# Optimization experiments

Measured on AMD Instinct MI355X. Metric: run time of the kernel, lower is better.

The kernel has to match this reference:

```python
import jax, jax.numpy as jnp
import numpy as np

DIM = 64
HEAD_DIM = 4
NUM_HEADS = DIM // HEAD_DIM  # 16
ATTN_DIM = NUM_HEADS * HEAD_DIM  # 64
BN_EPS = 1e-5


def setup_inputs() -> dict:
    key = jax.random.key(0)
    k_x, k_qkv, k_proj, k_g, k_b, k_m, k_v = jax.random.split(key, 7)
    B, C, H, W = 8, DIM, 64, 64
    x = jax.random.normal(k_x, (B, C, H, W), dtype=jnp.float32)
    # nn.Linear(dim, 3*attn_dim, bias=False): y = x @ W^T; store transposed for x @ w
    w_qkv = jax.random.normal(k_qkv, (DIM, 3 * ATTN_DIM), dtype=jnp.float32) * (DIM ** -0.5)
    w_proj = jax.random.normal(k_proj, (ATTN_DIM, DIM), dtype=jnp.float32) * (ATTN_DIM ** -0.5)
    gamma = 1.0 + 0.1 * jax.random.normal(k_g, (DIM,), dtype=jnp.float32)
    beta = 0.1 * jax.random.normal(k_b, (DIM,), dtype=jnp.float32)
    bn_mean = 0.1 * jax.random.normal(k_m, (DIM,), dtype=jnp.float32)
    bn_var = jnp.abs(jax.random.normal(k_v, (DIM,), dtype=jnp.float32)) + 0.5
    return {"x": x, "w_qkv": w_qkv, "w_proj": w_proj, "gamma": gamma,
            "beta": beta, "bn_mean": bn_mean, "bn_var": bn_var}


def _forward(x, w_qkv, w_proj, gamma, beta, bn_mean, bn_var):
    B, C, H, W = x.shape
    Hp, Wp = H // 2, W // 2
    N = Hp * Wp
    # ---- MaxPool2d(2,2) with indices (non-overlapping windows) ----
    xr = x.reshape(B, C, Hp, 2, Wp, 2).transpose(0, 1, 2, 4, 3, 5).reshape(B, C, Hp, Wp, 4)
    idx = jnp.argmax(xr, axis=-1)              # [B,C,Hp,Wp] window-local argmax
    pooled = jnp.max(xr, axis=-1)              # [B,C,Hp,Wp]
    # ---- GA attention on pooled map ----
    t = pooled.transpose(0, 2, 3, 1).reshape(B, N, C)          # [B,N,C]
    qkv = (t @ w_qkv).reshape(B, N, 3, NUM_HEADS, HEAD_DIM)
    q, k, v = qkv[:, :, 0], qkv[:, :, 1], qkv[:, :, 2]          # [B,N,h,d]
    scale = HEAD_DIM ** -0.5
    attn = jnp.einsum('bnhd,bmhd->bhnm', q, k) * scale          # [B,h,N,N]
    attn = jax.nn.softmax(attn, axis=-1)
    o = jnp.einsum('bhnm,bmhd->bnhd', attn, v).reshape(B, N, ATTN_DIM)
    o = (o @ w_proj).reshape(B, Hp, Wp, C).transpose(0, 3, 1, 2)  # [B,C,Hp,Wp]
    # ---- BatchNorm2d (eval mode, running stats) ----
    inv = gamma / jnp.sqrt(bn_var + BN_EPS)
    o = o * inv[:, None, None] + (beta - bn_mean * inv)[:, None, None]
    # ---- MaxUnpool2d(2,2): scatter to argmax positions ----
    oh = jax.nn.one_hot(idx, 4, dtype=o.dtype)                  # [B,C,Hp,Wp,4]
    up = oh * o[..., None]
    out = up.reshape(B, C, Hp, Wp, 2, 2).transpose(0, 1, 2, 4, 3, 5).reshape(B, C, H, W)
    return out


def reference(x, w_qkv, w_proj, gamma, beta, bn_mean, bn_var):
    return _forward(x, w_qkv, w_proj, gamma, beta, bn_mean, bn_var)
```

## Files before the change

kernel.cpp:

```cpp
#include <hip/hip_runtime.h>
#include <hip/hip_bf16.h>


typedef float    f32x4 __attribute__((ext_vector_type(4)));
typedef _Float16 f16x8 __attribute__((ext_vector_type(8)));
typedef unsigned int uint32_tt;

__global__ __launch_bounds__(256) void pool_kernel(const float* __restrict__ x,
                                                   float* __restrict__ t,
                                                   int* __restrict__ idx) {
    int g = blockIdx.x * 256 + threadIdx.x;
    int wp = g & 31, hp = (g >> 5) & 31, c = (g >> 10) & 63, b = g >> 16;
    const float* px = x + (((b * 64 + c) * 64 + 2 * hp) * 64 + 2 * wp);
    float2 r0 = *(const float2*)px;
    float2 r1 = *(const float2*)(px + 64);
    float best = r0.x; int bi = 0;
    if (r0.y > best) { best = r0.y; bi = 1; }
    if (r1.x > best) { best = r1.x; bi = 2; }
    if (r1.y > best) { best = r1.y; bi = 3; }
    int n = hp * 32 + wp;
    t[(b * 1024 + n) * 64 + c] = best;
    idx[g] = bi;
}

__global__ __launch_bounds__(192) void qkv_kernel(const float* __restrict__ t,
                                                  const float* __restrict__ w_qkv,
                                                  float* __restrict__ q,
                                                  float* __restrict__ k,
                                                  float* __restrict__ v) {
    __shared__ float trow[16 * 64];
    int tid = threadIdx.x;
    int row0 = blockIdx.x * 16;
    for (int i = tid; i < 1024; i += 192) trow[i] = t[row0 * 64 + i];
    int j  = tid % 96;
    int rh = tid / 96;
    float wc0[64], wc1[64];
    #pragma unroll
    for (int c = 0; c < 64; c++) {
        wc0[c] = w_qkv[c * 192 + j];
        wc1[c] = w_qkv[c * 192 + j + 96];
    }
    __syncthreads();
    int s0 = j >> 6, h0 = (j >> 2) & 15, d0 = j & 3;
    int j1 = j + 96;
    int s1 = j1 >> 6, h1 = (j1 >> 2) & 15, d1 = j1 & 3;
    float* dst0 = (s0 == 0) ? q : (s0 == 1) ? k : v;
    float* dst1 = (s1 == 0) ? q : (s1 == 1) ? k : v;
    for (int r = 0; r < 8; r++) {
        int row = rh * 8 + r;
        const float4* tr = (const float4*)&trow[row * 64];
        float a0 = 0.f, a1 = 0.f;
        #pragma unroll
        for (int c4 = 0; c4 < 16; c4++) {
            float4 tv = tr[c4];
            a0 += tv.x * wc0[c4 * 4] + tv.y * wc0[c4 * 4 + 1]
                + tv.z * wc0[c4 * 4 + 2] + tv.w * wc0[c4 * 4 + 3];
            a1 += tv.x * wc1[c4 * 4] + tv.y * wc1[c4 * 4 + 1]
                + tv.z * wc1[c4 * 4 + 2] + tv.w * wc1[c4 * 4 + 3];
        }
        int ng = row0 + row, b = ng >> 10, n = ng & 1023;
        dst0[((b * 16 + h0) * 1024 + n) * 4 + d0] = a0;
        dst1[((b * 16 + h1) * 1024 + n) * 4 + d1] = a1;
    }
}

__global__ __launch_bounds__(256) void attn_kernel(const float* __restrict__ q,
                                                   const float* __restrict__ k,
                                                   const float* __restrict__ v,
                                                   float* __restrict__ o) {
    __shared__ __align__(16) unsigned char smem[38080];
    f16x8*     Kh2 = (f16x8*)smem;
    uint32_tt* VT  = (uint32_tt*)(smem + 16384);
    float*     lsc = (float*)(smem + 37024);
    int bh = blockIdx.x >> 2;
    int row0 = (blockIdx.x & 3) * 256;
    int tid = threadIdx.x;
    const float4* kp4 = (const float4*)(k + bh * 4096);
    const float4* vp4 = (const float4*)(v + bh * 4096);
    #pragma unroll
    for (int i = 0; i < 4; i++) {
        int key = i * 256 + tid;
        float4 kf = kp4[key];
        f16x8 kk;
        kk[0] = (_Float16)kf.x; kk[4] = (_Float16)(kf.x - (float)kk[0]);
        kk[1] = (_Float16)kf.y; kk[5] = (_Float16)(kf.y - (float)kk[1]);
        kk[2] = (_Float16)kf.z; kk[6] = (_Float16)(kf.z - (float)kk[2]);
        kk[3] = (_Float16)kf.w; kk[7] = (_Float16)(kf.w - (float)kk[3]);
        Kh2[key] = kk;
        float4 vf = vp4[key];
        float vd[4] = { vf.x, vf.y, vf.z, vf.w };
        #pragma unroll
        for (int d = 0; d < 4; d++) {
            _Float16 h = (_Float16)vd[d];
            _Float16 l = (_Float16)(vd[d] - (float)h);
            uint32_tt hi = (uint32_tt)__builtin_bit_cast(unsigned short, l);
            uint32_tt lo = (uint32_tt)__builtin_bit_cast(unsigned short, h);
            VT[d * 1032 + key] = lo | (hi << 16);
        }
        VT[4 * 1032 + key] = 0x00003C00u;
    }
    int w = tid >> 6, lane = tid & 63;
    int c = lane & 15, quad = lane >> 4;
    int mv = (c < 5) ? c : 4;
    const float C1 = 0.5f * 1.44269504088896f;
    const float4* qp4 = (const float4*)(q + bh * 4096);
    f16x8 bq[4];
    #pragma unroll
    for (int s = 0; s < 4; s++) {
        int rowg = row0 + w * 64 + s * 16 + c;
        float4 qv = qp4[rowg];
        float qx = qv.x * C1, qy = qv.y * C1, qz = qv.z * C1, qw = qv.w * C1;
        _Float16 hx = (_Float16)qx, hy = (_Float16)qy,
                 hz = (_Float16)qz, hw = (_Float16)qw;
        _Float16 gx = (_Float16)(qx - (float)hx), gy = (_Float16)(qy - (float)hy),
                 gz = (_Float16)(qz - (float)hz), gw = (_Float16)(qw - (float)hw);
        f16x8 a = {};
        if (quad == 0) {
            a[0] = hx; a[1] = hy; a[2] = hz; a[3] = hw;
            a[4] = hx; a[5] = hy; a[6] = hz; a[7] = hw;
        } else if (quad == 1) {
            a[0] = gx; a[1] = gy; a[2] = gz; a[3] = gw;
            a[4] = gx; a[5] = gy; a[6] = gz; a[7] = gw;
        }
        bq[s] = a;
    }
    __syncthreads();
    f32x4 acc[4];
    #pragma unroll
    for (int s = 0; s < 4; s++) acc[s] = (f32x4)(0.f);
    #pragma unroll 2
    for (int t = 0; t < 64; t++) {
        f16x8 ka = Kh2[t * 16 + c];
        const uint32_tt* vp = &VT[mv * 1032 + t * 16 + quad * 4];
        uint4 vr = *(const uint4*)vp;
        f16x8 va = __builtin_bit_cast(f16x8, vr);
        #pragma unroll
        for (int s = 0; s < 4; s++) {
            f32x4 S = __builtin_amdgcn_mfma_f32_16x16x32_f16(ka, bq[s],
                                                             (f32x4)(0.f), 0, 0, 0);
            float p0 = __builtin_amdgcn_exp2f(S[0] - 14.f);
            float p1 = __builtin_amdgcn_exp2f(S[1] - 14.f);
            float p2 = __builtin_amdgcn_exp2f(S[2] - 14.f);
            float p3 = __builtin_amdgcn_exp2f(S[3] - 14.f);
            f16x8 pb = {};
            pb[0] = (_Float16)p0;
            pb[2] = (_Float16)p1;
            pb[4] = (_Float16)p2;
            pb[6] = (_Float16)p3;
            acc[s] = __builtin_amdgcn_mfma_f32_16x16x32_f16(va, pb, acc[s], 0, 0, 0);
        }
    }
    if (quad == 1) {
        #pragma unroll
        for (int s = 0; s < 4; s++) lsc[w * 64 + s * 16 + c] = acc[s][0];
    }
    __syncthreads();
    if (quad == 0) {
        int b0 = bh >> 4, h = bh & 15;
        #pragma unroll
        for (int s = 0; s < 4; s++) {
            float rl = 1.f / lsc[w * 64 + s * 16 + c];
            int rowg = row0 + w * 64 + s * 16 + c;
            float4 res = { acc[s][0] * rl, acc[s][1] * rl,
                           acc[s][2] * rl, acc[s][3] * rl };
            *(float4*)&o[(b0 * 1024 + rowg) * 64 + h * 4] = res;
        }
    }
}

__global__ __launch_bounds__(256) void proj_kernel(const float* __restrict__ o,
                                                   const float* __restrict__ w_proj,
                                                   const float* __restrict__ gamma,
                                                   const float* __restrict__ beta,
                                                   const float* __restrict__ mean,
                                                   const float* __restrict__ var,
                                                   const int* __restrict__ idx,
                                                   float* __restrict__ out) {
    __shared__ float ws[64 * 64];
    int b = blockIdx.x >> 5, hp = blockIdx.x & 31;
    int tid = threadIdx.x;
    for (int i = tid; i < 4096; i += 256) ws[i] = w_proj[i];
    int wp = tid & 31, cg = tid >> 5;
    float oreg[64];
    const float* orow = o + (b * 1024 + hp * 32 + wp) * 64;
    #pragma unroll
    for (int a4 = 0; a4 < 16; a4++) {
        float4 t4 = ((const float4*)orow)[a4];
        oreg[a4 * 4] = t4.x; oreg[a4 * 4 + 1] = t4.y;
        oreg[a4 * 4 + 2] = t4.z; oreg[a4 * 4 + 3] = t4.w;
    }
    __syncthreads();
    #pragma unroll
    for (int g = 0; g < 2; g++) {
        int c0 = cg * 8 + g * 4;
        float4 acc = {0.f, 0.f, 0.f, 0.f};
        #pragma unroll
        for (int a = 0; a < 64; a++) {
            float4 wv = *(const float4*)&ws[a * 64 + c0];
            acc.x += oreg[a] * wv.x; acc.y += oreg[a] * wv.y;
            acc.z += oreg[a] * wv.z; acc.w += oreg[a] * wv.w;
        }
        float accs[4] = { acc.x, acc.y, acc.z, acc.w };
        #pragma unroll
        for (int i = 0; i < 4; i++) {
            int c = c0 + i;
            float inv = gamma[c] * rsqrtf(var[c] + 1e-5f);
            float val = accs[i] * inv + (beta[c] - mean[c] * inv);
            int id = idx[((b * 64 + c) * 32 + hp) * 32 + wp];
            int base = ((b * 64 + c) * 64 + 2 * hp) * 64 + 2 * wp;
            float2 r0 = { id == 0 ? val : 0.f, id == 1 ? val : 0.f };
            float2 r1 = { id == 2 ? val : 0.f, id == 3 ? val : 0.f };
            *(float2*)&out[base] = r0;
            *(float2*)&out[base + 64] = r1;
        }
    }
}

extern "C" void kernel_launch(void* const* d_in, const int* in_sizes, int n_in,
                              void* d_out, int out_size, void* d_ws, size_t ws_size,
                              hipStream_t stream) {
    const float* x      = (const float*)d_in[0];
    const float* w_qkv  = (const float*)d_in[1];
    const float* w_proj = (const float*)d_in[2];
    const float* gamma  = (const float*)d_in[3];
    const float* beta   = (const float*)d_in[4];
    const float* bn_mean= (const float*)d_in[5];
    const float* bn_var = (const float*)d_in[6];
    float* out = (float*)d_out;

    const int SEG = 524288;
    float* ws = (float*)d_ws;
    float* t   = ws;
    int*   idx = (int*)(ws + SEG);
    float* q   = ws + 2 * SEG;
    float* k   = ws + 3 * SEG;
    float* v   = ws + 4 * SEG;
    float* o   = ws + 5 * SEG;

    pool_kernel<<<2048, 256, 0, stream>>>(x, t, idx);
    qkv_kernel<<<512, 192, 0, stream>>>(t, w_qkv, q, k, v);
    attn_kernel<<<512, 256, 0, stream>>>(q, k, v, o);
    proj_kernel<<<256, 256, 0, stream>>>(o, w_proj, gamma, beta, bn_mean, bn_var, idx, out);
}
```

Measured before the change: 129.8 us.

## Pack two key tiles per PV MFMA and drop split-fp16 V

Each PV MFMA now covers two 16-key tiles: the exponentiated scores from two QK MFMAs fill all eight fp16 slots of the operand, where before only four slots were used with hi/lo V pairs. V is stored as a single fp16 value in a permuted shared-memory layout to match, so the hi/lo split is dropped. This halves the number of PV MFMAs and the loop trip count, and shrinks shared memory. The cost is lower V precision (no fp16 residual term), which could push the result past tolerance.

```diff
diff --git a/kernel.cpp b/kernel.cpp
--- a/kernel.cpp
+++ b/kernel.cpp
@@ -68,10 +68,10 @@
                                                    const float* __restrict__ k,
                                                    const float* __restrict__ v,
                                                    float* __restrict__ o) {
-    __shared__ __align__(16) unsigned char smem[38080];
-    f16x8*     Kh2 = (f16x8*)smem;
-    uint32_tt* VT  = (uint32_tt*)(smem + 16384);
-    float*     lsc = (float*)(smem + 37024);
+    __shared__ __align__(16) unsigned char smem[27840];
+    f16x8*          Kh2 = (f16x8*)smem;
+    unsigned short* VTu = (unsigned short*)(smem + 16384);
+    float*          lsc = (float*)(smem + 26784);
     int bh = blockIdx.x >> 2;
     int row0 = (blockIdx.x & 3) * 256;
     int tid = threadIdx.x;
@@ -88,16 +88,13 @@
         kk[3] = (_Float16)kf.w; kk[7] = (_Float16)(kf.w - (float)kk[3]);
         Kh2[key] = kk;
         float4 vf = vp4[key];
-        float vd[4] = { vf.x, vf.y, vf.z, vf.w };
-        #pragma unroll
-        for (int d = 0; d < 4; d++) {
-            _Float16 h = (_Float16)vd[d];
-            _Float16 l = (_Float16)(vd[d] - (float)h);
-            uint32_tt hi = (uint32_tt)__builtin_bit_cast(unsigned short, l);
-            uint32_tt lo = (uint32_tt)__builtin_bit_cast(unsigned short, h);
-            VT[d * 1032 + key] = lo | (hi << 16);
-        }
-        VT[4 * 1032 + key] = 0x00003C00u;
+        int pos = (key & ~31) | (((key & 15) >> 2) << 3)
+                | (((key >> 4) & 1) << 2) | (key & 3);
+        VTu[0 * 1040 + pos] = __builtin_bit_cast(unsigned short, (_Float16)vf.x);
+        VTu[1 * 1040 + pos] = __builtin_bit_cast(unsigned short, (_Float16)vf.y);
+        VTu[2 * 1040 + pos] = __builtin_bit_cast(unsigned short, (_Float16)vf.z);
+        VTu[3 * 1040 + pos] = __builtin_bit_cast(unsigned short, (_Float16)vf.w);
+        VTu[4 * 1040 + key] = 0x3C00;
     }
     int w = tid >> 6, lane = tid & 63;
     int c = lane & 15, quad = lane >> 4;
@@ -129,24 +126,27 @@
     #pragma unroll
     for (int s = 0; s < 4; s++) acc[s] = (f32x4)(0.f);
     #pragma unroll 2
-    for (int t = 0; t < 64; t++) {
-        f16x8 ka = Kh2[t * 16 + c];
-        const uint32_tt* vp = &VT[mv * 1032 + t * 16 + quad * 4];
-        uint4 vr = *(const uint4*)vp;
-        f16x8 va = __builtin_bit_cast(f16x8, vr);
+    for (int T = 0; T < 32; T++) {
+        f16x8 ka0 = Kh2[(2 * T) * 16 + c];
+        f16x8 ka1 = Kh2[(2 * T + 1) * 16 + c];
+        const uint4* vptr = (const uint4*)((const unsigned char*)VTu
+                                           + mv * 2080 + T * 64 + quad * 16);
+        f16x8 va = __builtin_bit_cast(f16x8, *vptr);
         #pragma unroll
         for (int s = 0; s < 4; s++) {
-            f32x4 S = __builtin_amdgcn_mfma_f32_16x16x32_f16(ka, bq[s],
-                                                             (f32x4)(0.f), 0, 0, 0);
-            float p0 = __builtin_amdgcn_exp2f(S[0] - 14.f);
-            float p1 = __builtin_amdgcn_exp2f(S[1] - 14.f);
-            float p2 = __builtin_amdgcn_exp2f(S[2] - 14.f);
-            float p3 = __builtin_amdgcn_exp2f(S[3] - 14.f);
-            f16x8 pb = {};
-            pb[0] = (_Float16)p0;
-            pb[2] = (_Float16)p1;
-            pb[4] = (_Float16)p2;
-            pb[6] = (_Float16)p3;
+            f32x4 S0 = __builtin_amdgcn_mfma_f32_16x16x32_f16(ka0, bq[s],
+                                                              (f32x4)(0.f), 0, 0, 0);
+            f32x4 S1 = __builtin_amdgcn_mfma_f32_16x16x32_f16(ka1, bq[s],
+                                                              (f32x4)(0.f), 0, 0, 0);
+            f16x8 pb;
+            pb[0] = (_Float16)__builtin_amdgcn_exp2f(S0[0] - 14.f);
+            pb[1] = (_Float16)__builtin_amdgcn_exp2f(S0[1] - 14.f);
+            pb[2] = (_Float16)__builtin_amdgcn_exp2f(S0[2] - 14.f);
+            pb[3] = (_Float16)__builtin_amdgcn_exp2f(S0[3] - 14.f);
+            pb[4] = (_Float16)__builtin_amdgcn_exp2f(S1[0] - 14.f);
+            pb[5] = (_Float16)__builtin_amdgcn_exp2f(S1[1] - 14.f);
+            pb[6] = (_Float16)__builtin_amdgcn_exp2f(S1[2] - 14.f);
+            pb[7] = (_Float16)__builtin_amdgcn_exp2f(S1[3] - 14.f);
             acc[s] = __builtin_amdgcn_mfma_f32_16x16x32_f16(va, pb, acc[s], 0, 0, 0);
         }
     }
```

New measurement: 123.7 us. -4.7%, faster.
